# Kernel tuning notes

Hardware: AMD Instinct MI355X
Metric: run time of the kernel (lower is better)

## Reference

```python
import jax, jax.numpy as jnp
import numpy as np

BATCH, N_IN, N_MID, N_OUT = 1048576, 64, 32, 10


def setup_inputs() -> dict:
    key = jax.random.key(0)
    k_x, k_w1, k_b1, k_w2, k_b2 = jax.random.split(key, 5)
    # scalar synapse weights k collectively form dense matrices; init like
    # Synapse.init_weight: uniform(-sqrt(1/fan_in), sqrt(1/fan_in))
    v1 = np.sqrt(1.0 / N_IN)
    v2 = np.sqrt(1.0 / N_MID)
    return {
        "x": jax.random.normal(k_x, (BATCH, N_IN), dtype=jnp.float32),
        "W1": jax.random.uniform(k_w1, (N_IN, N_MID), dtype=jnp.float32, minval=-v1, maxval=v1),
        "b1": jnp.zeros((N_MID,), dtype=jnp.float32),  # obtain_float_parameter inits to 0.0
        "W2": jax.random.uniform(k_w2, (N_MID, N_OUT), dtype=jnp.float32, minval=-v2, maxval=v2),
        "b2": jnp.zeros((N_OUT,), dtype=jnp.float32),
    }


def reference(x, W1, b1, W2, b2):
    # RegularNeuron: output = ReLU(b + sum_j k_j * input_j)  -> relu(x @ W1 + b1)
    h = jax.nn.relu(x @ W1 + b1)  # [batch, n_middle]
    # DestinationNeuron (no activation): y = b + sum_j k_j * h_j -> h @ W2 + b2
    y = h @ W2 + b2  # [batch, n_outputs]
    return y
```

## Files before the change

### kernel.cpp

```cpp
#include <hip/hip_runtime.h>


#define N_IN  64
#define N_MID 32
#define N_OUT 10

#define WAVES_PER_BLOCK 4
#define TILES_PER_WAVE  8
#define ROWS_PER_TILE   16
#define ROWS_PER_BLOCK  (WAVES_PER_BLOCK * TILES_PER_WAVE * ROWS_PER_TILE)
#define NBUF            3
#define H_STRIDE        80
#define XTILE_BYTES     4096
#define ROW_BYTES       256

typedef short bf16x8 __attribute__((ext_vector_type(8)));
typedef float f32x4  __attribute__((ext_vector_type(4)));

typedef __attribute__((address_space(3))) unsigned char       lds_u8_as;
typedef const __attribute__((address_space(1))) unsigned char glb_u8_as;

static __device__ __forceinline__ short f2bf(float f) {
    __bf16 h = (__bf16)f;
    return __builtin_bit_cast(short, h);
}

static __device__ __forceinline__ unsigned pk2bf(float lo, float hi) {
    unsigned l = (unsigned short)__builtin_bit_cast(unsigned short, (__bf16)lo);
    unsigned h = (unsigned short)__builtin_bit_cast(unsigned short, (__bf16)hi);
    return (h << 16) | l;
}

__global__ __launch_bounds__(256)
void livenet_mfma(const float* __restrict__ x,
                  const float* __restrict__ W1,
                  const float* __restrict__ b1,
                  const float* __restrict__ W2,
                  const float* __restrict__ b2,
                  float* __restrict__ out,
                  int batch) {
    __shared__ __align__(16) unsigned char xstage_all[WAVES_PER_BLOCK][NBUF * XTILE_BYTES];
    __shared__ __align__(16) unsigned char h_lds_all[WAVES_PER_BLOCK][ROWS_PER_TILE * H_STRIDE];

    const int lane = threadIdx.x & 63;
    const int wave = threadIdx.x >> 6;
    const int g    = lane >> 4;
    const int c    = lane & 15;

    unsigned char* xstage = xstage_all[wave];
    unsigned char* h_lds  = h_lds_all[wave];

    bf16x8 w1f[2][2];
    #pragma unroll
    for (int n = 0; n < 2; ++n)
        #pragma unroll
        for (int p = 0; p < 2; ++p)
            #pragma unroll
            for (int i = 0; i < 8; ++i) {
                int k = p * 32 + 8 * g + i;
                w1f[n][p][i] = f2bf(W1[k * N_MID + n * 16 + c]);
            }

    bf16x8 w2f;
    #pragma unroll
    for (int i = 0; i < 8; ++i) {
        int kpos = 8 * g + i;
        int col  = (kpos & 1) * 16 + (kpos >> 1);
        w2f[i] = (c < N_OUT) ? f2bf(W2[col * N_OUT + c]) : (short)0;
    }

    const float b1v0 = b1[c];
    const float b1v1 = b1[16 + c];
    const float b2v  = (c < N_OUT) ? b2[c] : 0.0f;

    const int r_lo    = lane >> 4;
    const int mprime  = lane & 15;
    unsigned srcoff[4];
    #pragma unroll
    for (int j = 0; j < 4; ++j) {
        int r = 4 * j + r_lo;
        srcoff[j] = (unsigned)(r * ROW_BYTES + 16 * (mprime ^ (r & 7)));
    }

    const int cw = c & 7;
    const unsigned rd_a0lo = (unsigned)(c * ROW_BYTES + 16 * ((2 * g)     ^ cw));
    const unsigned rd_a0hi = (unsigned)(c * ROW_BYTES + 16 * ((2 * g + 1) ^ cw));
    const unsigned rd_a1lo = (unsigned)(c * ROW_BYTES + 16 * ((8 + 2 * g) ^ cw));
    const unsigned rd_a1hi = (unsigned)(c * ROW_BYTES + 16 * ((9 + 2 * g) ^ cw));

    const size_t wave_row0 = (size_t)blockIdx.x * ROWS_PER_BLOCK
                           + (size_t)wave * (TILES_PER_WAVE * ROWS_PER_TILE);
    const bool full = (wave_row0 + TILES_PER_WAVE * ROWS_PER_TILE) <= (size_t)batch;

    if (full) {
        const unsigned char* xb = (const unsigned char*)x + wave_row0 * ROW_BYTES;

        #pragma unroll
        for (int j = 0; j < 4; ++j) {
            __builtin_amdgcn_global_load_lds(
                (glb_u8_as*)(xb + srcoff[j]),
                (lds_u8_as*)(xstage + 0 * XTILE_BYTES + j * 1024), 16, 0, 0);
        }
        #pragma unroll
        for (int j = 0; j < 4; ++j) {
            __builtin_amdgcn_global_load_lds(
                (glb_u8_as*)(xb + XTILE_BYTES + srcoff[j]),
                (lds_u8_as*)(xstage + 1 * XTILE_BYTES + j * 1024), 16, 0, 0);
        }

        #pragma unroll
        for (int t = 0; t < TILES_PER_WAVE; ++t) {
            if (t + 2 < TILES_PER_WAVE) {
                const unsigned char* src = xb + (size_t)(t + 2) * XTILE_BYTES;
                unsigned char* nbuf = xstage + ((t + 2) % NBUF) * XTILE_BYTES;
                #pragma unroll
                for (int j = 0; j < 4; ++j) {
                    __builtin_amdgcn_global_load_lds(
                        (glb_u8_as*)(src + srcoff[j]),
                        (lds_u8_as*)(nbuf + j * 1024), 16, 0, 0);
                }
            }

            if (t == 0) {
                __asm__ volatile("s_waitcnt vmcnt(8)" ::: "memory");
            } else if (t == 1) {
                __asm__ volatile("s_waitcnt vmcnt(12)" ::: "memory");
            } else if (t == TILES_PER_WAVE - 2) {
                __asm__ volatile("s_waitcnt vmcnt(12)" ::: "memory");
            } else if (t == TILES_PER_WAVE - 1) {
                __asm__ volatile("s_waitcnt vmcnt(8)" ::: "memory");
            } else {
                __asm__ volatile("s_waitcnt vmcnt(16)" ::: "memory");
            }
            __builtin_amdgcn_sched_barrier(0);

            const unsigned char* xbuf = xstage + (t % NBUF) * XTILE_BYTES;

            const float4 f0 = *(const float4*)(xbuf + rd_a0lo);
            const float4 f1 = *(const float4*)(xbuf + rd_a0hi);
            const float4 f2 = *(const float4*)(xbuf + rd_a1lo);
            const float4 f3 = *(const float4*)(xbuf + rd_a1hi);

            bf16x8 a0, a1;
            a0[0] = f2bf(f0.x); a0[1] = f2bf(f0.y); a0[2] = f2bf(f0.z); a0[3] = f2bf(f0.w);
            a0[4] = f2bf(f1.x); a0[5] = f2bf(f1.y); a0[6] = f2bf(f1.z); a0[7] = f2bf(f1.w);
            a1[0] = f2bf(f2.x); a1[1] = f2bf(f2.y); a1[2] = f2bf(f2.z); a1[3] = f2bf(f2.w);
            a1[4] = f2bf(f3.x); a1[5] = f2bf(f3.y); a1[6] = f2bf(f3.z); a1[7] = f2bf(f3.w);

            f32x4 acc0 = {b1v0, b1v0, b1v0, b1v0};
            f32x4 acc1 = {b1v1, b1v1, b1v1, b1v1};
            acc0 = __builtin_amdgcn_mfma_f32_16x16x32_bf16(a0, w1f[0][0], acc0, 0, 0, 0);
            acc0 = __builtin_amdgcn_mfma_f32_16x16x32_bf16(a1, w1f[0][1], acc0, 0, 0, 0);
            acc1 = __builtin_amdgcn_mfma_f32_16x16x32_bf16(a0, w1f[1][0], acc1, 0, 0, 0);
            acc1 = __builtin_amdgcn_mfma_f32_16x16x32_bf16(a1, w1f[1][1], acc1, 0, 0, 0);

            #pragma unroll
            for (int r = 0; r < 4; ++r) {
                const int rowr = 4 * g + r;
                *(unsigned*)(h_lds + rowr * H_STRIDE + 4 * c) =
                    pk2bf(fmaxf(acc0[r], 0.0f), fmaxf(acc1[r], 0.0f));
            }
            __asm__ volatile("" ::: "memory");

            const bf16x8 hfrag = *(const bf16x8*)(h_lds + c * H_STRIDE + 16 * g);
            f32x4 acc2 = {b2v, b2v, b2v, b2v};
            acc2 = __builtin_amdgcn_mfma_f32_16x16x32_bf16(hfrag, w2f, acc2, 0, 0, 0);

            __asm__ volatile("" ::: "memory");

            if (c < N_OUT) {
                const size_t rb = wave_row0 + (size_t)t * ROWS_PER_TILE;
                float* op = out + (rb + 4 * g) * N_OUT + c;
                op[0 * N_OUT] = acc2[0];
                op[1 * N_OUT] = acc2[1];
                op[2 * N_OUT] = acc2[2];
                op[3 * N_OUT] = acc2[3];
            }
        }
    } else {
        for (int t = 0; t < TILES_PER_WAVE; ++t) {
            const size_t rb = wave_row0 + (size_t)t * ROWS_PER_TILE;
            if (rb + ROWS_PER_TILE > (size_t)batch) break;

            const float* xp = x + (rb + (size_t)c) * N_IN + 8 * g;
            float4 v0 = *(const float4*)(xp + 0);
            float4 v1 = *(const float4*)(xp + 4);
            float4 v2 = *(const float4*)(xp + 32);
            float4 v3 = *(const float4*)(xp + 36);

            bf16x8 a0, a1;
            a0[0] = f2bf(v0.x); a0[1] = f2bf(v0.y); a0[2] = f2bf(v0.z); a0[3] = f2bf(v0.w);
            a0[4] = f2bf(v1.x); a0[5] = f2bf(v1.y); a0[6] = f2bf(v1.z); a0[7] = f2bf(v1.w);
            a1[0] = f2bf(v2.x); a1[1] = f2bf(v2.y); a1[2] = f2bf(v2.z); a1[3] = f2bf(v2.w);
            a1[4] = f2bf(v3.x); a1[5] = f2bf(v3.y); a1[6] = f2bf(v3.z); a1[7] = f2bf(v3.w);

            f32x4 acc0 = {b1v0, b1v0, b1v0, b1v0};
            f32x4 acc1 = {b1v1, b1v1, b1v1, b1v1};
            acc0 = __builtin_amdgcn_mfma_f32_16x16x32_bf16(a0, w1f[0][0], acc0, 0, 0, 0);
            acc0 = __builtin_amdgcn_mfma_f32_16x16x32_bf16(a1, w1f[0][1], acc0, 0, 0, 0);
            acc1 = __builtin_amdgcn_mfma_f32_16x16x32_bf16(a0, w1f[1][0], acc1, 0, 0, 0);
            acc1 = __builtin_amdgcn_mfma_f32_16x16x32_bf16(a1, w1f[1][1], acc1, 0, 0, 0);

            #pragma unroll
            for (int r = 0; r < 4; ++r) {
                const int rowr = 4 * g + r;
                *(unsigned*)(h_lds + rowr * H_STRIDE + 4 * c) =
                    pk2bf(fmaxf(acc0[r], 0.0f), fmaxf(acc1[r], 0.0f));
            }
            __asm__ volatile("" ::: "memory");

            const bf16x8 hfrag = *(const bf16x8*)(h_lds + c * H_STRIDE + 16 * g);
            f32x4 acc2 = {b2v, b2v, b2v, b2v};
            acc2 = __builtin_amdgcn_mfma_f32_16x16x32_bf16(hfrag, w2f, acc2, 0, 0, 0);

            __asm__ volatile("" ::: "memory");

            if (c < N_OUT) {
                float* op = out + (rb + 4 * g) * N_OUT + c;
                op[0 * N_OUT] = acc2[0];
                op[1 * N_OUT] = acc2[1];
                op[2 * N_OUT] = acc2[2];
                op[3 * N_OUT] = acc2[3];
            }
        }
    }
}

extern "C" void kernel_launch(void* const* d_in, const int* in_sizes, int n_in,
                              void* d_out, int out_size, void* d_ws, size_t ws_size,
                              hipStream_t stream) {
    const float* x  = (const float*)d_in[0];
    const float* W1 = (const float*)d_in[1];
    const float* b1 = (const float*)d_in[2];
    const float* W2 = (const float*)d_in[3];
    const float* b2 = (const float*)d_in[4];
    float* out = (float*)d_out;

    int batch = in_sizes[0] / N_IN;
    int grid  = (batch + ROWS_PER_BLOCK - 1) / ROWS_PER_BLOCK;
    livenet_mfma<<<grid, 256, 0, stream>>>(x, W1, b1, W2, b2, out, batch);
}
```

Baseline: 61.20 us.

## Switch to persistent grid-stride waves with continuous triple-buffered prefetch

Replaces the fixed 8-tiles-per-wave block mapping with a fixed grid of 768 blocks whose waves stride over all 16-row tiles. The global-to-LDS triple-buffer pipeline now runs across many more tiles per wave, amortizing pipeline fill/drain and per-block weight setup. It drops the separate partial-tile path and relies on the batch being a multiple of 16; the fixed grid size may underfill or limit memory parallelism depending on occupancy.

```diff
diff --git a/kernel.cpp b/kernel.cpp
--- a/kernel.cpp
+++ b/kernel.cpp
@@ -6,9 +6,8 @@
 #define N_OUT 10
 
 #define WAVES_PER_BLOCK 4
-#define TILES_PER_WAVE  8
+#define GRID_BLOCKS     768
 #define ROWS_PER_TILE   16
-#define ROWS_PER_BLOCK  (WAVES_PER_BLOCK * TILES_PER_WAVE * ROWS_PER_TILE)
 #define NBUF            3
 #define H_STRIDE        80
 #define XTILE_BYTES     4096
@@ -88,141 +87,113 @@
     const unsigned rd_a1lo = (unsigned)(c * ROW_BYTES + 16 * ((8 + 2 * g) ^ cw));
     const unsigned rd_a1hi = (unsigned)(c * ROW_BYTES + 16 * ((9 + 2 * g) ^ cw));
 
-    const size_t wave_row0 = (size_t)blockIdx.x * ROWS_PER_BLOCK
-                           + (size_t)wave * (TILES_PER_WAVE * ROWS_PER_TILE);
-    const bool full = (wave_row0 + TILES_PER_WAVE * ROWS_PER_TILE) <= (size_t)batch;
-
-    if (full) {
-        const unsigned char* xb = (const unsigned char*)x + wave_row0 * ROW_BYTES;
-
+    const int GW         = GRID_BLOCKS * WAVES_PER_BLOCK;
+    const int gw         = blockIdx.x * WAVES_PER_BLOCK + wave;
+    const int ntile_tot  = batch / ROWS_PER_TILE;
+    const int n          = (ntile_tot > gw) ? (ntile_tot - gw + GW - 1) / GW : 0;
+
+    if (n == 0) return;
+
+    const unsigned char* xg = (const unsigned char*)x;
+    const size_t step = (size_t)GW * XTILE_BYTES;
+
+    {
+        const unsigned char* s0 = xg + (size_t)gw * XTILE_BYTES;
         #pragma unroll
         for (int j = 0; j < 4; ++j) {
             __builtin_amdgcn_global_load_lds(
-                (glb_u8_as*)(xb + srcoff[j]),
+                (glb_u8_as*)(s0 + srcoff[j]),
                 (lds_u8_as*)(xstage + 0 * XTILE_BYTES + j * 1024), 16, 0, 0);
         }
+        if (n > 1) {
+            const unsigned char* s1 = s0 + step;
+            #pragma unroll
+            for (int j = 0; j < 4; ++j) {
+                __builtin_amdgcn_global_load_lds(
+                    (glb_u8_as*)(s1 + srcoff[j]),
+                    (lds_u8_as*)(xstage + 1 * XTILE_BYTES + j * 1024), 16, 0, 0);
+            }
+        }
+    }
+
+    size_t off_c = (size_t)gw * XTILE_BYTES;
+    size_t off_s = off_c + 2 * step;
+    unsigned curb = 0;
+    unsigned stgb = 2 * XTILE_BYTES;
+    size_t   rb   = (size_t)gw * ROWS_PER_TILE;
+
+    for (int i = 0; i < n; ++i) {
+        if (i + 2 < n) {
+            const unsigned char* src = xg + off_s;
+            unsigned char* nbuf = xstage + stgb;
+            #pragma unroll
+            for (int j = 0; j < 4; ++j) {
+                __builtin_amdgcn_global_load_lds(
+                    (glb_u8_as*)(src + srcoff[j]),
+                    (lds_u8_as*)(nbuf + j * 1024), 16, 0, 0);
+            }
+        }
+
+        if (i == 0) {
+            __asm__ volatile("s_waitcnt vmcnt(8)" ::: "memory");
+        } else if (i == 1) {
+            __asm__ volatile("s_waitcnt vmcnt(12)" ::: "memory");
+        } else if (i == n - 1) {
+            __asm__ volatile("s_waitcnt vmcnt(8)" ::: "memory");
+        } else if (i == n - 2) {
+            __asm__ volatile("s_waitcnt vmcnt(12)" ::: "memory");
+        } else {
+            __asm__ volatile("s_waitcnt vmcnt(16)" ::: "memory");
+        }
+        __builtin_amdgcn_sched_barrier(0);
+
+        const unsigned char* xbuf = xstage + curb;
+
+        const float4 f0 = *(const float4*)(xbuf + rd_a0lo);
+        const float4 f1 = *(const float4*)(xbuf + rd_a0hi);
+        const float4 f2 = *(const float4*)(xbuf + rd_a1lo);
+        const float4 f3 = *(const float4*)(xbuf + rd_a1hi);
+
+        bf16x8 a0, a1;
+        a0[0] = f2bf(f0.x); a0[1] = f2bf(f0.y); a0[2] = f2bf(f0.z); a0[3] = f2bf(f0.w);
+        a0[4] = f2bf(f1.x); a0[5] = f2bf(f1.y); a0[6] = f2bf(f1.z); a0[7] = f2bf(f1.w);
+        a1[0] = f2bf(f2.x); a1[1] = f2bf(f2.y); a1[2] = f2bf(f2.z); a1[3] = f2bf(f2.w);
+        a1[4] = f2bf(f3.x); a1[5] = f2bf(f3.y); a1[6] = f2bf(f3.z); a1[7] = f2bf(f3.w);
+
+        f32x4 acc0 = {b1v0, b1v0, b1v0, b1v0};
+        f32x4 acc1 = {b1v1, b1v1, b1v1, b1v1};
+        acc0 = __builtin_amdgcn_mfma_f32_16x16x32_bf16(a0, w1f[0][0], acc0, 0, 0, 0);
+        acc0 = __builtin_amdgcn_mfma_f32_16x16x32_bf16(a1, w1f[0][1], acc0, 0, 0, 0);
+        acc1 = __builtin_amdgcn_mfma_f32_16x16x32_bf16(a0, w1f[1][0], acc1, 0, 0, 0);
+        acc1 = __builtin_amdgcn_mfma_f32_16x16x32_bf16(a1, w1f[1][1], acc1, 0, 0, 0);
+
         #pragma unroll
-        for (int j = 0; j < 4; ++j) {
-            __builtin_amdgcn_global_load_lds(
-                (glb_u8_as*)(xb + XTILE_BYTES + srcoff[j]),
-                (lds_u8_as*)(xstage + 1 * XTILE_BYTES + j * 1024), 16, 0, 0);
-        }
-
-        #pragma unroll
-        for (int t = 0; t < TILES_PER_WAVE; ++t) {
-            if (t + 2 < TILES_PER_WAVE) {
-                const unsigned char* src = xb + (size_t)(t + 2) * XTILE_BYTES;
-                unsigned char* nbuf = xstage + ((t + 2) % NBUF) * XTILE_BYTES;
-                #pragma unroll
-                for (int j = 0; j < 4; ++j) {
-                    __builtin_amdgcn_global_load_lds(
-                        (glb_u8_as*)(src + srcoff[j]),
-                        (lds_u8_as*)(nbuf + j * 1024), 16, 0, 0);
-                }
-            }
-
-            if (t == 0) {
-                __asm__ volatile("s_waitcnt vmcnt(8)" ::: "memory");
-            } else if (t == 1) {
-                __asm__ volatile("s_waitcnt vmcnt(12)" ::: "memory");
-            } else if (t == TILES_PER_WAVE - 2) {
-                __asm__ volatile("s_waitcnt vmcnt(12)" ::: "memory");
-            } else if (t == TILES_PER_WAVE - 1) {
-                __asm__ volatile("s_waitcnt vmcnt(8)" ::: "memory");
-            } else {
-                __asm__ volatile("s_waitcnt vmcnt(16)" ::: "memory");
-            }
-            __builtin_amdgcn_sched_barrier(0);
-
-            const unsigned char* xbuf = xstage + (t % NBUF) * XTILE_BYTES;
-
-            const float4 f0 = *(const float4*)(xbuf + rd_a0lo);
-            const float4 f1 = *(const float4*)(xbuf + rd_a0hi);
-            const float4 f2 = *(const float4*)(xbuf + rd_a1lo);
-            const float4 f3 = *(const float4*)(xbuf + rd_a1hi);
-
-            bf16x8 a0, a1;
-            a0[0] = f2bf(f0.x); a0[1] = f2bf(f0.y); a0[2] = f2bf(f0.z); a0[3] = f2bf(f0.w);
-            a0[4] = f2bf(f1.x); a0[5] = f2bf(f1.y); a0[6] = f2bf(f1.z); a0[7] = f2bf(f1.w);
-            a1[0] = f2bf(f2.x); a1[1] = f2bf(f2.y); a1[2] = f2bf(f2.z); a1[3] = f2bf(f2.w);
-            a1[4] = f2bf(f3.x); a1[5] = f2bf(f3.y); a1[6] = f2bf(f3.z); a1[7] = f2bf(f3.w);
-
-            f32x4 acc0 = {b1v0, b1v0, b1v0, b1v0};
-            f32x4 acc1 = {b1v1, b1v1, b1v1, b1v1};
-            acc0 = __builtin_amdgcn_mfma_f32_16x16x32_bf16(a0, w1f[0][0], acc0, 0, 0, 0);
-            acc0 = __builtin_amdgcn_mfma_f32_16x16x32_bf16(a1, w1f[0][1], acc0, 0, 0, 0);
-            acc1 = __builtin_amdgcn_mfma_f32_16x16x32_bf16(a0, w1f[1][0], acc1, 0, 0, 0);
-            acc1 = __builtin_amdgcn_mfma_f32_16x16x32_bf16(a1, w1f[1][1], acc1, 0, 0, 0);
-
-            #pragma unroll
-            for (int r = 0; r < 4; ++r) {
-                const int rowr = 4 * g + r;
-                *(unsigned*)(h_lds + rowr * H_STRIDE + 4 * c) =
-                    pk2bf(fmaxf(acc0[r], 0.0f), fmaxf(acc1[r], 0.0f));
-            }
-            __asm__ volatile("" ::: "memory");
-
-            const bf16x8 hfrag = *(const bf16x8*)(h_lds + c * H_STRIDE + 16 * g);
-            f32x4 acc2 = {b2v, b2v, b2v, b2v};
-            acc2 = __builtin_amdgcn_mfma_f32_16x16x32_bf16(hfrag, w2f, acc2, 0, 0, 0);
-
-            __asm__ volatile("" ::: "memory");
-
-            if (c < N_OUT) {
-                const size_t rb = wave_row0 + (size_t)t * ROWS_PER_TILE;
-                float* op = out + (rb + 4 * g) * N_OUT + c;
-                op[0 * N_OUT] = acc2[0];
-                op[1 * N_OUT] = acc2[1];
-                op[2 * N_OUT] = acc2[2];
-                op[3 * N_OUT] = acc2[3];
-            }
-        }
-    } else {
-        for (int t = 0; t < TILES_PER_WAVE; ++t) {
-            const size_t rb = wave_row0 + (size_t)t * ROWS_PER_TILE;
-            if (rb + ROWS_PER_TILE > (size_t)batch) break;
-
-            const float* xp = x + (rb + (size_t)c) * N_IN + 8 * g;
-            float4 v0 = *(const float4*)(xp + 0);
-            float4 v1 = *(const float4*)(xp + 4);
-            float4 v2 = *(const float4*)(xp + 32);
-            float4 v3 = *(const float4*)(xp + 36);
-
-            bf16x8 a0, a1;
-            a0[0] = f2bf(v0.x); a0[1] = f2bf(v0.y); a0[2] = f2bf(v0.z); a0[3] = f2bf(v0.w);
-            a0[4] = f2bf(v1.x); a0[5] = f2bf(v1.y); a0[6] = f2bf(v1.z); a0[7] = f2bf(v1.w);
-            a1[0] = f2bf(v2.x); a1[1] = f2bf(v2.y); a1[2] = f2bf(v2.z); a1[3] = f2bf(v2.w);
-            a1[4] = f2bf(v3.x); a1[5] = f2bf(v3.y); a1[6] = f2bf(v3.z); a1[7] = f2bf(v3.w);
-
-            f32x4 acc0 = {b1v0, b1v0, b1v0, b1v0};
-            f32x4 acc1 = {b1v1, b1v1, b1v1, b1v1};
-            acc0 = __builtin_amdgcn_mfma_f32_16x16x32_bf16(a0, w1f[0][0], acc0, 0, 0, 0);
-            acc0 = __builtin_amdgcn_mfma_f32_16x16x32_bf16(a1, w1f[0][1], acc0, 0, 0, 0);
-            acc1 = __builtin_amdgcn_mfma_f32_16x16x32_bf16(a0, w1f[1][0], acc1, 0, 0, 0);
-            acc1 = __builtin_amdgcn_mfma_f32_16x16x32_bf16(a1, w1f[1][1], acc1, 0, 0, 0);
-
-            #pragma unroll
-            for (int r = 0; r < 4; ++r) {
-                const int rowr = 4 * g + r;
-                *(unsigned*)(h_lds + rowr * H_STRIDE + 4 * c) =
-                    pk2bf(fmaxf(acc0[r], 0.0f), fmaxf(acc1[r], 0.0f));
-            }
-            __asm__ volatile("" ::: "memory");
-
-            const bf16x8 hfrag = *(const bf16x8*)(h_lds + c * H_STRIDE + 16 * g);
-            f32x4 acc2 = {b2v, b2v, b2v, b2v};
-            acc2 = __builtin_amdgcn_mfma_f32_16x16x32_bf16(hfrag, w2f, acc2, 0, 0, 0);
-
-            __asm__ volatile("" ::: "memory");
-
-            if (c < N_OUT) {
-                float* op = out + (rb + 4 * g) * N_OUT + c;
-                op[0 * N_OUT] = acc2[0];
-                op[1 * N_OUT] = acc2[1];
-                op[2 * N_OUT] = acc2[2];
-                op[3 * N_OUT] = acc2[3];
-            }
-        }
+        for (int r = 0; r < 4; ++r) {
+            const int rowr = 4 * g + r;
+            *(unsigned*)(h_lds + rowr * H_STRIDE + 4 * c) =
+                pk2bf(fmaxf(acc0[r], 0.0f), fmaxf(acc1[r], 0.0f));
+        }
+        __asm__ volatile("" ::: "memory");
+
+        const bf16x8 hfrag = *(const bf16x8*)(h_lds + c * H_STRIDE + 16 * g);
+        f32x4 acc2 = {b2v, b2v, b2v, b2v};
+        acc2 = __builtin_amdgcn_mfma_f32_16x16x32_bf16(hfrag, w2f, acc2, 0, 0, 0);
+
+        __asm__ volatile("" ::: "memory");
+
+        if (c < N_OUT) {
+            float* op = out + (rb + 4 * g) * N_OUT + c;
+            op[0 * N_OUT] = acc2[0];
+            op[1 * N_OUT] = acc2[1];
+            op[2 * N_OUT] = acc2[2];
+            op[3 * N_OUT] = acc2[3];
+        }
+
+        off_c += step;
+        off_s += step;
+        rb    += (size_t)GW * ROWS_PER_TILE;
+        curb += XTILE_BYTES; if (curb == NBUF * XTILE_BYTES) curb = 0;
+        stgb += XTILE_BYTES; if (stgb == NBUF * XTILE_BYTES) stgb = 0;
     }
 }
 
@@ -237,6 +208,5 @@
     float* out = (float*)d_out;
 
     int batch = in_sizes[0] / N_IN;
-    int grid  = (batch + ROWS_PER_BLOCK - 1) / ROWS_PER_BLOCK;
-    livenet_mfma<<<grid, 256, 0, stream>>>(x, W1, b1, W2, b2, out, batch);
-}
+    livenet_mfma<<<GRID_BLOCKS, 256, 0, stream>>>(x, W1, b1, W2, b2, out, batch);
+}
```

After: 67.79 us. +10.8%, slower.
